# Performance work log

Measured on AMD Instinct MI355X. Metric: run time of the kernel, lower is better.

Reference implementation:

```python
import jax, jax.numpy as jnp
import numpy as np


def _conv3x3(x, w, b):
    # x: [B,C,H,W], w: [O,C,3,3], b: [O]; stride 1, padding 1 (SAME)
    y = jax.lax.conv_general_dilated(
        x, w,
        window_strides=(1, 1),
        padding=((1, 1), (1, 1)),
        dimension_numbers=("NCHW", "OIHW", "NCHW"),
    )
    return y + b[None, :, None, None]


def setup_inputs() -> dict:
    key = jax.random.key(0)
    k_x, k_w1, k_b1, k_w2, k_b2 = jax.random.split(key, 5)
    B, Cin, H, W = 16, 128, 96, 96
    Ch = 256
    # Kaiming-ish small init for conv weights
    x = jax.random.normal(k_x, (B, Cin, H, W), dtype=jnp.float32)
    w1 = jax.random.normal(k_w1, (Ch, Cin, 3, 3), dtype=jnp.float32) * (1.0 / np.sqrt(Cin * 9))
    b1 = jax.random.normal(k_b1, (Ch,), dtype=jnp.float32) * 0.01
    w2 = jax.random.normal(k_w2, (2, Ch, 3, 3), dtype=jnp.float32) * (1.0 / np.sqrt(Ch * 9))
    b2 = jax.random.normal(k_b2, (2,), dtype=jnp.float32) * 0.01
    return {"x": x, "w1": w1, "b1": b1, "w2": w2, "b2": b2}


def reference(x, w1, b1, w2, b2):
    # DeformConv2d with zero offsets == plain 3x3 conv (stride 1, pad 1) + bias.
    h = jax.nn.relu(_conv3x3(x, w1, b1))  # [B,256,H,W]
    return _conv3x3(h, w2, b2)            # [B,2,H,W]
```

## Files before the change

### kernel.cpp

```cpp
#include <hip/hip_runtime.h>
#include <stdint.h>

typedef unsigned short ushort_t;
typedef __attribute__((ext_vector_type(8))) short short8;
typedef __attribute__((ext_vector_type(4))) float floatx4;
typedef __attribute__((ext_vector_type(4))) unsigned short ushortx4;
typedef __attribute__((ext_vector_type(8))) unsigned short ushortx8;

#define B_   16
#define CIN  128
#define CH   256
#define HW   96
#define HP   98

#define XPAD_ELEMS (B_*HP*HP*CIN)
#define HPAD_ELEMS (B_*HP*HP*CH)
#define XPAD_OFF 0
#define HPAD_OFF (XPAD_ELEMS*2)
#define W1T_OFF  (HPAD_OFF + HPAD_ELEMS*2)
#define W2T_OFF  (W1T_OFF + 256*1152*2)

__device__ __forceinline__ ushort_t f2bf(float f){
  uint32_t u = __float_as_uint(f);
  u += 0x7FFF + ((u >> 16) & 1);
  return (ushort_t)(u >> 16);
}
__device__ __forceinline__ float bf2f(ushort_t h){
  return __uint_as_float(((uint32_t)h) << 16);
}
__device__ __forceinline__ void async_ld16(void* lds, const void* g){
  __builtin_amdgcn_global_load_lds(
      (const __attribute__((address_space(1))) void*)g,
      (__attribute__((address_space(3))) void*)lds, 16, 0, 0);
}

__global__ void zero_border(uint32_t* __restrict__ base, int C2){
  int tid = blockIdx.x*256 + threadIdx.x;
  int perimg = 388*C2;
  int total = B_*perimg;
  if (tid >= total) return;
  int b = tid / perimg; int r = tid % perimg;
  int cell = r / C2;    int cu = r % C2;
  int y, x;
  if      (cell < 98)  { y = 0;            x = cell;       }
  else if (cell < 196) { y = 97;           x = cell - 98;  }
  else if (cell < 292) { y = cell - 195;   x = 0;          }
  else                 { y = cell - 291;   x = 97;         }
  base[((b*HP + y)*HP + x)*C2 + cu] = 0u;
}

__global__ void transform_x(const float* __restrict__ x, ushort_t* __restrict__ xpad){
  __shared__ float lds[32][33];
  int bid = blockIdx.x;
  int ct = bid & 3; int xt = (bid>>2) % 3; int yt = (bid/12) % 24; int b = bid/288;
  int c0 = ct*32, x0 = xt*32, y0 = yt*4;
  int t = threadIdx.x;
  for (int yy=0; yy<4; ++yy){
    int y = y0 + yy;
    #pragma unroll
    for (int rep=0; rep<4; ++rep){
      int idx = rep*256 + t;
      int ci = idx >> 5, xj = idx & 31;
      lds[ci][xj] = x[((b*CIN + c0+ci)*HW + y)*HW + x0 + xj];
    }
    __syncthreads();
    int px = t >> 3, quad = t & 7;
    ushortx4 v;
    #pragma unroll
    for (int k=0;k<4;k++) v[k] = f2bf(lds[quad*4+k][px]);
    *(ushortx4*)&xpad[(((b*HP + y+1)*HP) + x0+px+1)*CIN + c0 + quad*4] = v;
    __syncthreads();
  }
}

__global__ void transform_w1(const float* __restrict__ w1, ushort_t* __restrict__ w1t){
  int tid = blockIdx.x*256 + threadIdx.x;
  int o = tid / 1152, k = tid - o*1152;
  int tap = k >> 7, c = k & 127;
  w1t[tid] = f2bf(w1[(o*CIN + c)*9 + tap]);
}

__global__ void transform_w2(const float* __restrict__ w2, float* __restrict__ w2t){
  int tid = blockIdx.x*256 + threadIdx.x;
  if (tid >= 4608) return;
  int ch = tid & 1, c = (tid >> 1) & 255, tap = tid >> 9;
  w2t[tid] = w2[(ch*CH + c)*9 + tap];
}

#define C1_TILE(KT, VMN, SB) { \
  asm volatile("s_waitcnt vmcnt(" #VMN ")" ::: "memory"); \
  __builtin_amdgcn_s_barrier(); \
  __builtin_amdgcn_sched_barrier(0); \
  const int kt_ = (KT); \
  { const int ka_ = kt_ + 1; \
    if (ka_ < 18) { \
      const int ab_ = (ka_ & 1) * 16384; \
      _Pragma("unroll") \
      for (int j=0;j<4;++j) \
        async_ld16(&Alds[ab_ + j*4096 + adst], &w1t[asrc + j*73728 + ka_*64]); \
    } } \
  if (SB) { \
    const int kb_ = kt_ + 2; \
    const int tapb_ = kb_ >> 1; \
    const int dyb_ = tapb_/3; const int dxb_ = tapb_ - dyb_*3; \
    const int bdb_ = (dyb_*HP + dxb_)*CIN + (kb_&1)*64; \
    const int bb_ = (kb_ % 3) * 12288; \
    _Pragma("unroll") \
    for (int j=0;j<3;++j) \
      async_ld16(&Blds[bb_ + j*4096 + bdst], &xpad[bsrc + j*(2*HP*CIN) + bdb_]); \
  } \
  const ushort_t* Ab = &Alds[(kt_ & 1) * 16384]; \
  const ushort_t* Bb = &Blds[(kt_ % 3) * 12288]; \
  short8 bb0[3], aa0[4], aa1[4], bb1[3], cc0[4], cc1[4]; \
  _Pragma("unroll") \
  for (int nf=0; nf<3; ++nf) bb0[nf] = *(const short8*)&Bb[bbase_r + nf*1024 + koff0]; \
  _Pragma("unroll") \
  for (int mf=0; mf<4; ++mf) aa0[mf] = *(const short8*)&Ab[abase_r + mf*1024 + koff0]; \
  _Pragma("unroll") \
  for (int mf=0; mf<4; ++mf) aa1[mf] = *(const short8*)&Ab[abase_r + (mf+4)*1024 + koff0]; \
  __builtin_amdgcn_s_setprio(1); \
  _Pragma("unroll") \
  for (int mf=0; mf<4; ++mf) \
    _Pragma("unroll") \
    for (int nf=0; nf<3; ++nf) \
      acc[mf][nf] = __builtin_amdgcn_mfma_f32_16x16x32_bf16(aa0[mf], bb0[nf], acc[mf][nf], 0,0,0); \
  __builtin_amdgcn_s_setprio(0); \
  _Pragma("unroll") \
  for (int nf=0; nf<3; ++nf) bb1[nf] = *(const short8*)&Bb[bbase_r + nf*1024 + koff1]; \
  _Pragma("unroll") \
  for (int mf=0; mf<4; ++mf) cc0[mf] = *(const short8*)&Ab[abase_r + mf*1024 + koff1]; \
  __builtin_amdgcn_s_setprio(1); \
  _Pragma("unroll") \
  for (int mf=0; mf<4; ++mf) \
    _Pragma("unroll") \
    for (int nf=0; nf<3; ++nf) \
      acc[mf+4][nf] = __builtin_amdgcn_mfma_f32_16x16x32_bf16(aa1[mf], bb0[nf], acc[mf+4][nf], 0,0,0); \
  __builtin_amdgcn_s_setprio(0); \
  _Pragma("unroll") \
  for (int mf=0; mf<4; ++mf) cc1[mf] = *(const short8*)&Ab[abase_r + (mf+4)*1024 + koff1]; \
  __builtin_amdgcn_s_setprio(1); \
  _Pragma("unroll") \
  for (int mf=0; mf<4; ++mf) \
    _Pragma("unroll") \
    for (int nf=0; nf<3; ++nf) \
      acc[mf][nf] = __builtin_amdgcn_mfma_f32_16x16x32_bf16(cc0[mf], bb1[nf], acc[mf][nf], 0,0,0); \
  _Pragma("unroll") \
  for (int mf=0; mf<4; ++mf) \
    _Pragma("unroll") \
    for (int nf=0; nf<3; ++nf) \
      acc[mf+4][nf] = __builtin_amdgcn_mfma_f32_16x16x32_bf16(cc1[mf], bb1[nf], acc[mf+4][nf], 0,0,0); \
  __builtin_amdgcn_s_setprio(0); \
}

__global__ __launch_bounds__(512, 1) void conv1(const ushort_t* __restrict__ xpad,
                                                const ushort_t* __restrict__ w1t,
                                                const float* __restrict__ b1,
                                                ushort_t* __restrict__ hpad){
  __shared__ __align__(16) ushort_t Alds[2*16384];
  __shared__ __align__(16) ushort_t Blds[3*12288];
  int orig = blockIdx.x;
  int bid = (orig & 7) * 96 + (orig >> 3);
  int b = bid / 48; int rem = bid - b*48;
  int y0 = (rem/3)*6, x0 = (rem - (rem/3)*3)*32;
  int t = threadIdx.x;
  int lane = t & 63, wave = t >> 6;
  int wm = wave & 1, wn = wave >> 1;
  int r = lane & 15, q = lane >> 4;

  const int arow0 = t >> 3;
  const int soct  = (t & 7) ^ (arow0 & 7);
  const int adst  = t * 8;
  const int asrc  = arow0 * 1152 + soct * 8;
  const int bty0  = arow0 >> 5, btx0 = arow0 & 31;
  const int bdst  = t * 8;
  const int bsrc  = ((b*HP + y0 + bty0)*HP + x0 + btx0)*CIN + soct * 8;

  const int koff0 = ((0*4 + q) ^ (r & 7)) * 8;
  const int koff1 = ((1*4 + q) ^ (r & 7)) * 8;
  const int abase_r = (wm*128 + r) * 64;
  const int bbase_r = (wn*48  + r) * 64;

  floatx4 acc[8][3];
  #pragma unroll
  for (int i=0;i<8;i++)
    #pragma unroll
    for (int j=0;j<3;j++) acc[i][j] = (floatx4){0.f,0.f,0.f,0.f};

  #pragma unroll
  for (int j=0;j<3;++j) async_ld16(&Blds[0     + j*4096 + bdst], &xpad[bsrc + j*(2*HP*CIN)]);
  #pragma unroll
  for (int j=0;j<4;++j) async_ld16(&Alds[0     + j*4096 + adst], &w1t[asrc + j*73728]);
  #pragma unroll
  for (int j=0;j<3;++j) async_ld16(&Blds[12288 + j*4096 + bdst], &xpad[bsrc + j*(2*HP*CIN) + 64]);

  for (int kt=0; kt<16; ++kt){
    C1_TILE(kt, 3, 1)
  }
  C1_TILE(16, 3, 0)
  C1_TILE(17, 0, 0)

  #pragma unroll
  for (int mf=0; mf<8; ++mf){
    int o = wm*128 + mf*16 + q*4;
    float bias0 = b1[o], bias1 = b1[o+1], bias2 = b1[o+2], bias3 = b1[o+3];
    #pragma unroll
    for (int nf=0; nf<3; ++nf){
      int n = wn*48 + nf*16 + r;
      int ty = n >> 5, tx = n & 31;
      ushortx4 v;
      v[0] = f2bf(fmaxf(acc[mf][nf][0] + bias0, 0.f));
      v[1] = f2bf(fmaxf(acc[mf][nf][1] + bias1, 0.f));
      v[2] = f2bf(fmaxf(acc[mf][nf][2] + bias2, 0.f));
      v[3] = f2bf(fmaxf(acc[mf][nf][3] + bias3, 0.f));
      *(ushortx4*)&hpad[((b*HP + y0+ty+1)*HP + (x0+tx+1))*CH + o] = v;
    }
  }
}

__global__ __launch_bounds__(256) void conv2(const ushort_t* __restrict__ hpad,
                                             const float* __restrict__ w2t,
                                             const float* __restrict__ b2,
                                             float* __restrict__ out){
  __shared__ __align__(16) ushort_t hlds[25600];
  __shared__ float part[4][64][2];
  int bid = blockIdx.x;
  int b = bid / 144; int rem = bid - b*144;
  int yt = rem / 12, xt = rem - yt*12;
  int y0 = yt*8, x0 = xt*8;
  int t = threadIdx.x;
  int wave = t >> 6, lane = t & 63;

  for (int pass=0; pass<13; ++pass){
    int u = pass*256 + t;
    if (u < 3200){
      int cell = u >> 5, cf = u & 31;
      int hy = cell / 10, hx = cell - hy*10;
      const ushort_t* src = hpad + ((b*HP + y0+hy)*HP + (x0+hx))*CH
                                 + ((cf ^ (cell & 7)) << 3);
      async_ld16(&hlds[(pass*256 + wave*64)*8], src);
    }
  }
  __syncthreads();

  int q = __builtin_amdgcn_readfirstlane(wave);
  int ty = lane >> 3, tx = lane & 7;
  float a0 = 0.f, a1 = 0.f;
  for (int tap=0; tap<9; ++tap){
    int dy = tap/3, dxx = tap - dy*3;
    int cell = (ty+dy)*10 + (tx+dxx);
    int s = cell & 7;
    const float* wp = w2t + (tap*256 + q*64)*2;
    #pragma unroll
    for (int g=0; g<8; ++g){
      int j = q*8 + g;
      ushortx8 hv = *(const ushortx8*)&hlds[cell*256 + ((j ^ s) << 3)];
      #pragma unroll
      for (int i=0;i<8;i++){
        float hf = bf2f(hv[i]);
        a0 = fmaf(hf, wp[(g*8+i)*2    ], a0);
        a1 = fmaf(hf, wp[(g*8+i)*2 + 1], a1);
      }
    }
  }
  part[wave][lane][0] = a0;
  part[wave][lane][1] = a1;
  __syncthreads();
  if (t < 128){
    int sel = t >> 6, pix = t & 63;
    float v = part[0][pix][sel] + part[1][pix][sel]
            + part[2][pix][sel] + part[3][pix][sel] + b2[sel];
    int yy = y0 + (pix >> 3), xx = x0 + (pix & 7);
    out[(b*2 + sel)*9216 + yy*96 + xx] = v;
  }
}

extern "C" void kernel_launch(void* const* d_in, const int* in_sizes, int n_in,
                              void* d_out, int out_size, void* d_ws, size_t ws_size,
                              hipStream_t stream){
  const float* x  = (const float*)d_in[0];
  const float* w1 = (const float*)d_in[1];
  const float* b1 = (const float*)d_in[2];
  const float* w2 = (const float*)d_in[3];
  const float* b2 = (const float*)d_in[4];
  float* out = (float*)d_out;
  char* ws = (char*)d_ws;
  ushort_t* xpad = (ushort_t*)(ws + XPAD_OFF);
  ushort_t* hpad = (ushort_t*)(ws + HPAD_OFF);
  ushort_t* w1t  = (ushort_t*)(ws + W1T_OFF);
  float*    w2t  = (float*)(ws + W2T_OFF);

  hipLaunchKernelGGL(zero_border, dim3(16*388*64/256),  dim3(256), 0, stream, (uint32_t*)xpad, 64);
  hipLaunchKernelGGL(zero_border, dim3(16*388*128/256), dim3(256), 0, stream, (uint32_t*)hpad, 128);
  hipLaunchKernelGGL(transform_x,  dim3(4608),  dim3(256), 0, stream, x, xpad);
  hipLaunchKernelGGL(transform_w1, dim3(1152),  dim3(256), 0, stream, w1, w1t);
  hipLaunchKernelGGL(transform_w2, dim3(18),    dim3(256), 0, stream, w2, w2t);
  hipLaunchKernelGGL(conv1, dim3(768),  dim3(512), 0, stream, xpad, w1t, b1, hpad);
  hipLaunchKernelGGL(conv2, dim3(2304), dim3(256), 0, stream, hpad, w2t, b2, out);
}
```

Measured before the change: 177.3 us.

## Split conv1 K-tile into four barrier-separated phases interleaving loads with MFMA

Restructures each conv1 K-tile into four phases. Each phase issues its LDS fragment reads plus a slice of the next tile's global-to-LDS async copies, then waits on lgkmcnt and runs its MFMA cluster between workgroup barriers, so memory traffic is spread across the MFMA work instead of being issued in a burst at the start. This adds several extra s_barrier and waitcnt points per tile, which could add synchronisation stalls. Register pressure may also shift because fragment loads are deferred.

```diff
diff --git a/kernel.cpp b/kernel.cpp
--- a/kernel.cpp
+++ b/kernel.cpp
@@ -87,63 +87,94 @@
   w2t[tid] = w2[(ch*CH + c)*9 + tap];
 }
 
-#define C1_TILE(KT, VMN, SB) { \
+#define C1_TILE(KT, VMN, SA, SB) { \
   asm volatile("s_waitcnt vmcnt(" #VMN ")" ::: "memory"); \
   __builtin_amdgcn_s_barrier(); \
   __builtin_amdgcn_sched_barrier(0); \
   const int kt_ = (KT); \
-  { const int ka_ = kt_ + 1; \
-    if (ka_ < 18) { \
-      const int ab_ = (ka_ & 1) * 16384; \
-      _Pragma("unroll") \
-      for (int j=0;j<4;++j) \
-        async_ld16(&Alds[ab_ + j*4096 + adst], &w1t[asrc + j*73728 + ka_*64]); \
-    } } \
+  const ushort_t* Ab = &Alds[(kt_ & 1) * 16384]; \
+  const ushort_t* Bb = &Blds[(kt_ % 3) * 12288]; \
+  short8 aa0[4], aa1[4], bb0[3], bb1[3], cc0[4], cc1[4]; \
+   \
+  _Pragma("unroll") \
+  for (int nf=0; nf<3; ++nf) bb0[nf] = *(const short8*)&Bb[bbase_r + nf*1024 + koff0]; \
+  _Pragma("unroll") \
+  for (int mf=0; mf<4; ++mf) aa0[mf] = *(const short8*)&Ab[abase_r + mf*1024 + koff0]; \
+  if (SA) { \
+    const int ka_ = kt_ + 1; const int ab_ = (ka_ & 1) * 16384; \
+    async_ld16(&Alds[ab_ +     0 + adst], &w1t[asrc +       0 + ka_*64]); \
+    async_ld16(&Alds[ab_ +  4096 + adst], &w1t[asrc +   73728 + ka_*64]); \
+  } \
+  __builtin_amdgcn_s_barrier(); \
+  asm volatile("s_waitcnt lgkmcnt(0)" ::: "memory"); \
+  __builtin_amdgcn_sched_barrier(0); \
+  __builtin_amdgcn_s_setprio(1); \
+  _Pragma("unroll") \
+  for (int mf=0; mf<4; ++mf) \
+    _Pragma("unroll") \
+    for (int nf=0; nf<3; ++nf) \
+      acc[mf][nf] = __builtin_amdgcn_mfma_f32_16x16x32_bf16(aa0[mf], bb0[nf], acc[mf][nf], 0,0,0); \
+  __builtin_amdgcn_s_setprio(0); \
+  __builtin_amdgcn_s_barrier(); \
+   \
+  _Pragma("unroll") \
+  for (int mf=0; mf<4; ++mf) aa1[mf] = *(const short8*)&Ab[abase_r + (mf+4)*1024 + koff0]; \
+  if (SA) { \
+    const int ka_ = kt_ + 1; const int ab_ = (ka_ & 1) * 16384; \
+    async_ld16(&Alds[ab_ +  8192 + adst], &w1t[asrc + 2*73728 + ka_*64]); \
+    async_ld16(&Alds[ab_ + 12288 + adst], &w1t[asrc + 3*73728 + ka_*64]); \
+  } \
+  __builtin_amdgcn_s_barrier(); \
+  asm volatile("s_waitcnt lgkmcnt(0)" ::: "memory"); \
+  __builtin_amdgcn_sched_barrier(0); \
+  __builtin_amdgcn_s_setprio(1); \
+  _Pragma("unroll") \
+  for (int mf=0; mf<4; ++mf) \
+    _Pragma("unroll") \
+    for (int nf=0; nf<3; ++nf) \
+      acc[mf+4][nf] = __builtin_amdgcn_mfma_f32_16x16x32_bf16(aa1[mf], bb0[nf], acc[mf+4][nf], 0,0,0); \
+  __builtin_amdgcn_s_setprio(0); \
+  __builtin_amdgcn_s_barrier(); \
+   \
+  _Pragma("unroll") \
+  for (int nf=0; nf<3; ++nf) bb1[nf] = *(const short8*)&Bb[bbase_r + nf*1024 + koff1]; \
+  _Pragma("unroll") \
+  for (int mf=0; mf<4; ++mf) cc0[mf] = *(const short8*)&Ab[abase_r + mf*1024 + koff1]; \
   if (SB) { \
     const int kb_ = kt_ + 2; \
     const int tapb_ = kb_ >> 1; \
     const int dyb_ = tapb_/3; const int dxb_ = tapb_ - dyb_*3; \
     const int bdb_ = (dyb_*HP + dxb_)*CIN + (kb_&1)*64; \
     const int bb_ = (kb_ % 3) * 12288; \
-    _Pragma("unroll") \
-    for (int j=0;j<3;++j) \
-      async_ld16(&Blds[bb_ + j*4096 + bdst], &xpad[bsrc + j*(2*HP*CIN) + bdb_]); \
+    async_ld16(&Blds[bb_ +    0 + bdst], &xpad[bsrc +            bdb_]); \
+    async_ld16(&Blds[bb_ + 4096 + bdst], &xpad[bsrc + 2*HP*CIN + bdb_]); \
   } \
-  const ushort_t* Ab = &Alds[(kt_ & 1) * 16384]; \
-  const ushort_t* Bb = &Blds[(kt_ % 3) * 12288]; \
-  short8 bb0[3], aa0[4], aa1[4], bb1[3], cc0[4], cc1[4]; \
-  _Pragma("unroll") \
-  for (int nf=0; nf<3; ++nf) bb0[nf] = *(const short8*)&Bb[bbase_r + nf*1024 + koff0]; \
-  _Pragma("unroll") \
-  for (int mf=0; mf<4; ++mf) aa0[mf] = *(const short8*)&Ab[abase_r + mf*1024 + koff0]; \
-  _Pragma("unroll") \
-  for (int mf=0; mf<4; ++mf) aa1[mf] = *(const short8*)&Ab[abase_r + (mf+4)*1024 + koff0]; \
-  __builtin_amdgcn_s_setprio(1); \
-  _Pragma("unroll") \
-  for (int mf=0; mf<4; ++mf) \
-    _Pragma("unroll") \
-    for (int nf=0; nf<3; ++nf) \
-      acc[mf][nf] = __builtin_amdgcn_mfma_f32_16x16x32_bf16(aa0[mf], bb0[nf], acc[mf][nf], 0,0,0); \
-  __builtin_amdgcn_s_setprio(0); \
-  _Pragma("unroll") \
-  for (int nf=0; nf<3; ++nf) bb1[nf] = *(const short8*)&Bb[bbase_r + nf*1024 + koff1]; \
-  _Pragma("unroll") \
-  for (int mf=0; mf<4; ++mf) cc0[mf] = *(const short8*)&Ab[abase_r + mf*1024 + koff1]; \
-  __builtin_amdgcn_s_setprio(1); \
-  _Pragma("unroll") \
-  for (int mf=0; mf<4; ++mf) \
-    _Pragma("unroll") \
-    for (int nf=0; nf<3; ++nf) \
-      acc[mf+4][nf] = __builtin_amdgcn_mfma_f32_16x16x32_bf16(aa1[mf], bb0[nf], acc[mf+4][nf], 0,0,0); \
-  __builtin_amdgcn_s_setprio(0); \
-  _Pragma("unroll") \
-  for (int mf=0; mf<4; ++mf) cc1[mf] = *(const short8*)&Ab[abase_r + (mf+4)*1024 + koff1]; \
+  __builtin_amdgcn_s_barrier(); \
+  asm volatile("s_waitcnt lgkmcnt(0)" ::: "memory"); \
+  __builtin_amdgcn_sched_barrier(0); \
   __builtin_amdgcn_s_setprio(1); \
   _Pragma("unroll") \
   for (int mf=0; mf<4; ++mf) \
     _Pragma("unroll") \
     for (int nf=0; nf<3; ++nf) \
       acc[mf][nf] = __builtin_amdgcn_mfma_f32_16x16x32_bf16(cc0[mf], bb1[nf], acc[mf][nf], 0,0,0); \
+  __builtin_amdgcn_s_setprio(0); \
+  __builtin_amdgcn_s_barrier(); \
+   \
+  _Pragma("unroll") \
+  for (int mf=0; mf<4; ++mf) cc1[mf] = *(const short8*)&Ab[abase_r + (mf+4)*1024 + koff1]; \
+  if (SB) { \
+    const int kb_ = kt_ + 2; \
+    const int tapb_ = kb_ >> 1; \
+    const int dyb_ = tapb_/3; const int dxb_ = tapb_ - dyb_*3; \
+    const int bdb_ = (dyb_*HP + dxb_)*CIN + (kb_&1)*64; \
+    const int bb_ = (kb_ % 3) * 12288; \
+    async_ld16(&Blds[bb_ + 8192 + bdst], &xpad[bsrc + 4*HP*CIN + bdb_]); \
+  } \
+  __builtin_amdgcn_s_barrier(); \
+  asm volatile("s_waitcnt lgkmcnt(0)" ::: "memory"); \
+  __builtin_amdgcn_sched_barrier(0); \
+  __builtin_amdgcn_s_setprio(1); \
   _Pragma("unroll") \
   for (int mf=0; mf<4; ++mf) \
     _Pragma("unroll") \
@@ -194,10 +225,10 @@
   for (int j=0;j<3;++j) async_ld16(&Blds[12288 + j*4096 + bdst], &xpad[bsrc + j*(2*HP*CIN) + 64]);
 
   for (int kt=0; kt<16; ++kt){
-    C1_TILE(kt, 3, 1)
-  }
-  C1_TILE(16, 3, 0)
-  C1_TILE(17, 0, 0)
+    C1_TILE(kt, 3, 1, 1)
+  }
+  C1_TILE(16, 3, 1, 0)
+  C1_TILE(17, 0, 0, 0)
 
   #pragma unroll
   for (int mf=0; mf<8; ++mf){
```

Measured after the change: 174.5 us. About the same (-1.6%).
